# Kernel tuning notes

Hardware: AMD Instinct MI355X
Metric: run time of the kernel (lower is better)

The kernel has to match this reference:

```python
import jax, jax.numpy as jnp
import numpy as np

TEMPERATURE = 0.07
EPS = 1e-8
LAMBDA_CONTRASTIVE = 0.3
AMBIGUOUS_THRESHOLD = 0.05
LABEL_SMOOTHING = 0.1

B, D, NUM_DIMS, NUM_PIECES = 4096, 256, 19, 1024


def setup_inputs() -> dict:
    key = jax.random.key(0)
    ks = jax.random.split(key, 7)
    return {
        "z_a": jax.random.normal(ks[0], (B, D), dtype=jnp.float32),
        "z_b": jax.random.normal(ks[1], (B, D), dtype=jnp.float32),
        "ranking_logits": jax.random.normal(ks[2], (B, NUM_DIMS), dtype=jnp.float32),
        "labels_a": jax.random.uniform(ks[3], (B, NUM_DIMS), dtype=jnp.float32),
        "labels_b": jax.random.uniform(ks[4], (B, NUM_DIMS), dtype=jnp.float32),
        "piece_ids_a": jax.random.randint(ks[5], (B,), 0, NUM_PIECES, dtype=jnp.int64 if jax.config.jax_enable_x64 else jnp.int32),
        "piece_ids_b": jax.random.randint(ks[6], (B,), 0, NUM_PIECES, dtype=jnp.int64 if jax.config.jax_enable_x64 else jnp.int32),
    }


def _infonce(embeddings, piece_ids, temperature=TEMPERATURE, eps=EPS):
    # embeddings [N, D], piece_ids [N]. Same-piece samples are positives.
    norm = jnp.sqrt(jnp.sum(embeddings * embeddings, axis=-1, keepdims=True))
    z = embeddings / jnp.maximum(norm, eps)  # F.normalize semantics
    sim = (z @ z.T) / temperature  # [N, N]
    n = sim.shape[0]
    eye = jnp.eye(n, dtype=bool)
    piece_mask = piece_ids[None, :] == piece_ids[:, None]
    pos_mask = piece_mask & ~eye
    neg_mask = (~piece_mask) & ~eye
    # row-wise max subtraction (detached in torch) is a no-op on the value since
    # (pos - logsumexp) is shift-invariant; compute stably via masked logsumexp.
    neg_inf = jnp.array(-jnp.inf, sim.dtype)
    neg_lse = jax.scipy.special.logsumexp(jnp.where(neg_mask, sim, neg_inf), axis=-1)  # [N]
    valid_anchor = pos_mask.any(axis=1) & neg_mask.any(axis=1)  # [N]
    pair_mask = pos_mask & valid_anchor[:, None]  # each positive of a valid anchor
    # per-positive term: logsumexp([pos_sim, negs_of_row]) - pos_sim
    lse = jnp.logaddexp(sim, neg_lse[:, None])  # [N, N]
    term = jnp.where(pair_mask, lse - sim, 0.0)
    count = jnp.sum(pair_mask)
    loss = jnp.sum(term) / jnp.maximum(count, 1)
    return jnp.where(count > 0, loss, 0.0)


def _ranking_loss(logits, labels_a, labels_b,
                  ambiguous_threshold=AMBIGUOUS_THRESHOLD,
                  label_smoothing=LABEL_SMOOTHING):
    label_diff = labels_a - labels_b
    targets = (label_diff > 0).astype(logits.dtype)
    non_ambiguous = jnp.abs(label_diff) >= ambiguous_threshold
    targets = targets * (1.0 - label_smoothing) + 0.5 * label_smoothing
    # BCE-with-logits, elementwise, mean over non-ambiguous entries
    bce = jnp.maximum(logits, 0.0) - logits * targets + jnp.log1p(jnp.exp(-jnp.abs(logits)))
    cnt = jnp.sum(non_ambiguous)
    loss = jnp.sum(jnp.where(non_ambiguous, bce, 0.0)) / jnp.maximum(cnt, 1)
    return jnp.where(cnt > 0, loss, 0.0)


def reference(z_a, z_b, ranking_logits, labels_a, labels_b, piece_ids_a, piece_ids_b):
    l_rank = _ranking_loss(ranking_logits, labels_a, labels_b)
    all_z = jnp.concatenate([z_a, z_b], axis=0)        # [2B, D]
    all_pieces = jnp.concatenate([piece_ids_a, piece_ids_b], axis=0)  # [2B]
    l_contrast = _infonce(all_z, all_pieces)
    total = l_rank + LAMBDA_CONTRASTIVE * l_contrast
    return (total, l_rank, l_contrast)
```

## Files before the change

### kernel.cpp

```cpp
#include <hip/hip_runtime.h>
#include <hip/hip_bf16.h>
#include <math.h>

#define NTOT 8192
#define HB   4096
#define DIM  256
#define RANK_N (4096*19)
#define INV_T 14.285714285714286f
#define SHIFT 16.0f
#define MAXP  48

typedef __attribute__((ext_vector_type(8))) short bf16x8_t;
typedef __attribute__((ext_vector_type(4))) float f32x4_t;

__device__ __forceinline__ unsigned short f2bf(float f) {
  union { float fv; unsigned int u; } v; v.fv = f;
  unsigned int u = v.u;
  unsigned int r = u + 0x7FFFu + ((u >> 16) & 1u);
  return (unsigned short)(r >> 16);
}

__device__ __forceinline__ const float* zrow(const float* za, const float* zb, int g) {
  return g < HB ? za + (size_t)g * DIM : zb + (size_t)(g - HB) * DIM;
}
__device__ __forceinline__ int piece_of(const int* pa, const int* pb, int g) {
  return g < HB ? pa[g] : pb[g - HB];
}

__global__ void k_norm(const float* __restrict__ za, const float* __restrict__ zb,
                       const int* __restrict__ pa, const int* __restrict__ pb,
                       unsigned short* __restrict__ zn, int* __restrict__ hist) {
  int lane = threadIdx.x & 63;
  int w = threadIdx.x >> 6;
  int row = blockIdx.x * 4 + w;
  const float* src = zrow(za, zb, row);
  float4 v = *reinterpret_cast<const float4*>(src + lane * 4);
  float ss = v.x * v.x + v.y * v.y + v.z * v.z + v.w * v.w;
  for (int o = 32; o; o >>= 1) ss += __shfl_xor(ss, o, 64);
  float inv = 1.0f / fmaxf(sqrtf(ss), 1e-8f);
  ushort4 o;
  o.x = f2bf(v.x * inv); o.y = f2bf(v.y * inv);
  o.z = f2bf(v.z * inv); o.w = f2bf(v.w * inv);
  *reinterpret_cast<ushort4*>(zn + (size_t)row * DIM + lane * 4) = o;
  if (lane == 0) atomicAdd(&hist[piece_of(pa, pb, row)], 1);
}

__global__ void k_rank(const float* __restrict__ logits, const float* __restrict__ la,
                       const float* __restrict__ lb, float* __restrict__ accf) {
  int e = blockIdx.x * 256 + threadIdx.x;
  float lsum = 0.f, lcnt = 0.f;
  float diff = la[e] - lb[e];
  if (fabsf(diff) >= 0.05f) {
    float x = logits[e];
    float tgt = diff > 0.f ? 0.95f : 0.05f;
    lsum = fmaxf(x, 0.f) - x * tgt + log1pf(__expf(-fabsf(x)));
    lcnt = 1.f;
  }
  for (int o = 32; o; o >>= 1) { lsum += __shfl_xor(lsum, o, 64); lcnt += __shfl_xor(lcnt, o, 64); }
  __shared__ float sred[8];
  int w = threadIdx.x >> 6, lane = threadIdx.x & 63;
  if (lane == 0) { sred[w * 2] = lsum; sred[w * 2 + 1] = lcnt; }
  __syncthreads();
  if (threadIdx.x == 0) {
    float S = 0.f, C = 0.f;
    for (int i = 0; i < 4; ++i) { S += sred[i * 2]; C += sred[i * 2 + 1]; }
    atomicAdd(&accf[0], S);
    atomicAdd(&accf[1], C);
  }
}

__global__ __launch_bounds__(256, 2)
void k_gram(const unsigned short* __restrict__ zn,
            const int* __restrict__ pa, const int* __restrict__ pb,
            float* __restrict__ neg_s, int* __restrict__ posCount,
            float* __restrict__ pos_sims) {
  __shared__ unsigned short Bs[64 * 264];
  const int t = threadIdx.x;
  const int lane = t & 63;
  const int w = t >> 6;
  const int l15 = lane & 15;
  const int lg = lane >> 4;
  const int it = blockIdx.x >> 3;
  const int chunk = blockIdx.x & 7;
  const int ibase = it * 128;
  const int jbase0 = chunk * 1024;

  bf16x8_t afrag[2][8];
  for (int mt = 0; mt < 2; ++mt) {
    int garow = ibase + w * 32 + mt * 16 + l15;
    const unsigned short* asrc = zn + (size_t)garow * DIM;
    for (int ks = 0; ks < 8; ++ks)
      afrag[mt][ks] = *reinterpret_cast<const bf16x8_t*>(asrc + lg * 8 + ks * 32);
  }

  int prow[8], irow[8];
  for (int mt = 0; mt < 2; ++mt)
    for (int r = 0; r < 4; ++r) {
      int g = ibase + w * 32 + mt * 16 + lg * 4 + r;
      irow[mt * 4 + r] = g;
      prow[mt * 4 + r] = piece_of(pa, pb, g);
    }

  float s[8] = {0.f, 0.f, 0.f, 0.f, 0.f, 0.f, 0.f, 0.f};

  for (int jt = 0; jt < 16; ++jt) {
    int jb = jbase0 + jt * 64;
    __syncthreads();
    for (int i = 0; i < 8; ++i) {
      int f = t + i * 256;
      int r = f >> 5;
      int c = f & 31;
      bf16x8_t v = *reinterpret_cast<const bf16x8_t*>(zn + (size_t)(jb + r) * DIM + c * 8);
      *reinterpret_cast<bf16x8_t*>(&Bs[r * 264 + c * 8]) = v;
    }
    __syncthreads();
    for (int ct = 0; ct < 4; ++ct) {
      int jj = jb + ct * 16 + l15;
      int pc = piece_of(pa, pb, jj);
      int brow = ct * 16 + l15;
      f32x4_t acc0 = {0.f, 0.f, 0.f, 0.f};
      f32x4_t acc1 = {0.f, 0.f, 0.f, 0.f};
      for (int ks = 0; ks < 8; ++ks) {
        bf16x8_t bfrag = *reinterpret_cast<const bf16x8_t*>(&Bs[brow * 264 + lg * 8 + ks * 32]);
        acc0 = __builtin_amdgcn_mfma_f32_16x16x32_bf16(afrag[0][ks], bfrag, acc0, 0, 0, 0);
        acc1 = __builtin_amdgcn_mfma_f32_16x16x32_bf16(afrag[1][ks], bfrag, acc1, 0, 0, 0);
      }
      for (int r = 0; r < 4; ++r) {
        float sim0 = acc0[r] * INV_T;
        if (pc != prow[r]) {
          s[r] += __expf(sim0 - SHIFT);
        } else if (jj != irow[r]) {
          int slot = atomicAdd(&posCount[irow[r]], 1);
          if (slot < MAXP) pos_sims[(size_t)irow[r] * MAXP + slot] = sim0;
        }
        float sim1 = acc1[r] * INV_T;
        if (pc != prow[4 + r]) {
          s[4 + r] += __expf(sim1 - SHIFT);
        } else if (jj != irow[4 + r]) {
          int slot = atomicAdd(&posCount[irow[4 + r]], 1);
          if (slot < MAXP) pos_sims[(size_t)irow[4 + r] * MAXP + slot] = sim1;
        }
      }
    }
  }
  for (int q = 0; q < 8; ++q) {
    float v = s[q];
    v += __shfl_xor(v, 1, 64);
    v += __shfl_xor(v, 2, 64);
    v += __shfl_xor(v, 4, 64);
    v += __shfl_xor(v, 8, 64);
    if (l15 == 0) atomicAdd(&neg_s[irow[q]], v);
  }
}

__global__ void k_pos2(const int* __restrict__ pa, const int* __restrict__ pb,
                       const int* __restrict__ hist, const float* __restrict__ neg_s,
                       const int* __restrict__ posCount, const float* __restrict__ pos_sims,
                       float* __restrict__ accf) {
  int i = blockIdx.x * 256 + threadIdx.x;
  float lsum = 0.f, lcnt = 0.f;
  int pi = piece_of(pa, pb, i);
  int cnt = hist[pi];
  if (cnt - 1 > 0 && NTOT - cnt > 0) {
    float nlse = SHIFT + logf(neg_s[i]);
    int m = posCount[i];
    if (m > MAXP) m = MAXP;
    for (int s = 0; s < m; ++s) {
      float sim = pos_sims[(size_t)i * MAXP + s];
      float x = nlse - sim;
      lsum += fmaxf(x, 0.f) + log1pf(__expf(-fabsf(x)));
    }
    lcnt = (float)(cnt - 1);
  }
  for (int o = 32; o; o >>= 1) { lsum += __shfl_xor(lsum, o, 64); lcnt += __shfl_xor(lcnt, o, 64); }
  int lane = threadIdx.x & 63;
  if (lane == 0) {
    atomicAdd(&accf[2], lsum);
    atomicAdd(&accf[3], lcnt);
  }
}

__global__ void k_final(const float* __restrict__ accf, float* __restrict__ out) {
  float rs = accf[0], rc = accf[1], ps = accf[2], pc = accf[3];
  float l_rank = rc > 0.f ? rs / rc : 0.f;
  float l_con = pc > 0.f ? ps / pc : 0.f;
  out[0] = l_rank + 0.3f * l_con;
  out[1] = l_rank;
  out[2] = l_con;
}

extern "C" void kernel_launch(void* const* d_in, const int* in_sizes, int n_in,
                              void* d_out, int out_size, void* d_ws, size_t ws_size,
                              hipStream_t stream) {
  const float* za     = (const float*)d_in[0];
  const float* zb     = (const float*)d_in[1];
  const float* logits = (const float*)d_in[2];
  const float* la     = (const float*)d_in[3];
  const float* lb     = (const float*)d_in[4];
  const int*   pa     = (const int*)d_in[5];
  const int*   pb     = (const int*)d_in[6];
  float* out = (float*)d_out;

  float* wsf = (float*)d_ws;
  int*   wsi = (int*)d_ws;
  float* neg_s    = wsf + 4;
  int*   hist     = wsi + 4 + NTOT;
  int*   posCount = wsi + 4 + NTOT + 1024;
  float* pos_sims = wsf + 4 + NTOT + 1024 + NTOT;
  unsigned short* zn = (unsigned short*)(wsf + 4 + NTOT + 1024 + NTOT + (size_t)NTOT * MAXP);

  hipMemsetAsync(d_ws, 0, (size_t)(4 + NTOT + 1024 + NTOT) * 4, stream);
  k_norm<<<NTOT / 4, 256, 0, stream>>>(za, zb, pa, pb, zn, hist);
  k_rank<<<RANK_N / 256, 256, 0, stream>>>(logits, la, lb, wsf);
  k_gram<<<512, 256, 0, stream>>>(zn, pa, pb, neg_s, posCount, pos_sims);
  k_pos2<<<NTOT / 256, 256, 0, stream>>>(pa, pb, hist, neg_s, posCount, pos_sims, wsf);
  k_final<<<1, 1, 0, stream>>>(wsf, out);
}
```

Before: 189.6 us.

## Merge small kernels, swizzle LDS, cache piece ids, double gram grid

Fuses the norm and ranking kernels into one launch, and merges the positive-pair reduction with the final combine into a single one-block kernel, cutting five launches to three. The gram kernel now splits columns into 16 chunks so it launches 1024 blocks, with launch bounds raised to 4 blocks per CU. Its LDS tile drops the padding in favour of an XOR swizzle, and column piece ids are cached in shared memory instead of read from global memory per tile. It also recomputes row indices instead of holding them in registers. The post kernel runs in one block and loops serially over 8192 rows, which may cost more than it saves.

After: 377.9 us. +99.3%, slower.

```diff
diff --git a/kernel.cpp b/kernel.cpp
--- a/kernel.cpp
+++ b/kernel.cpp
@@ -6,6 +6,8 @@
 #define HB   4096
 #define DIM  256
 #define RANK_N (4096*19)
+#define NORM_BLOCKS (NTOT/4)
+#define RANK_BLOCKS (RANK_N/256)
 #define INV_T 14.285714285714286f
 #define SHIFT 16.0f
 #define MAXP  48
@@ -27,63 +29,70 @@
   return g < HB ? pa[g] : pb[g - HB];
 }
 
-__global__ void k_norm(const float* __restrict__ za, const float* __restrict__ zb,
-                       const int* __restrict__ pa, const int* __restrict__ pb,
-                       unsigned short* __restrict__ zn, int* __restrict__ hist) {
-  int lane = threadIdx.x & 63;
-  int w = threadIdx.x >> 6;
-  int row = blockIdx.x * 4 + w;
-  const float* src = zrow(za, zb, row);
-  float4 v = *reinterpret_cast<const float4*>(src + lane * 4);
-  float ss = v.x * v.x + v.y * v.y + v.z * v.z + v.w * v.w;
-  for (int o = 32; o; o >>= 1) ss += __shfl_xor(ss, o, 64);
-  float inv = 1.0f / fmaxf(sqrtf(ss), 1e-8f);
-  ushort4 o;
-  o.x = f2bf(v.x * inv); o.y = f2bf(v.y * inv);
-  o.z = f2bf(v.z * inv); o.w = f2bf(v.w * inv);
-  *reinterpret_cast<ushort4*>(zn + (size_t)row * DIM + lane * 4) = o;
-  if (lane == 0) atomicAdd(&hist[piece_of(pa, pb, row)], 1);
-}
-
-__global__ void k_rank(const float* __restrict__ logits, const float* __restrict__ la,
-                       const float* __restrict__ lb, float* __restrict__ accf) {
-  int e = blockIdx.x * 256 + threadIdx.x;
-  float lsum = 0.f, lcnt = 0.f;
-  float diff = la[e] - lb[e];
-  if (fabsf(diff) >= 0.05f) {
-    float x = logits[e];
-    float tgt = diff > 0.f ? 0.95f : 0.05f;
-    lsum = fmaxf(x, 0.f) - x * tgt + log1pf(__expf(-fabsf(x)));
-    lcnt = 1.f;
-  }
-  for (int o = 32; o; o >>= 1) { lsum += __shfl_xor(lsum, o, 64); lcnt += __shfl_xor(lcnt, o, 64); }
+__global__ void k_pre(const float* __restrict__ za, const float* __restrict__ zb,
+                      const float* __restrict__ logits, const float* __restrict__ la,
+                      const float* __restrict__ lb,
+                      const int* __restrict__ pa, const int* __restrict__ pb,
+                      unsigned short* __restrict__ zn, int* __restrict__ hist,
+                      float* __restrict__ accf) {
   __shared__ float sred[8];
-  int w = threadIdx.x >> 6, lane = threadIdx.x & 63;
-  if (lane == 0) { sred[w * 2] = lsum; sred[w * 2 + 1] = lcnt; }
-  __syncthreads();
-  if (threadIdx.x == 0) {
-    float S = 0.f, C = 0.f;
-    for (int i = 0; i < 4; ++i) { S += sred[i * 2]; C += sred[i * 2 + 1]; }
-    atomicAdd(&accf[0], S);
-    atomicAdd(&accf[1], C);
-  }
-}
-
-__global__ __launch_bounds__(256, 2)
+  int bid = blockIdx.x;
+  int t = threadIdx.x;
+  if (bid < NORM_BLOCKS) {
+    int lane = t & 63, w = t >> 6;
+    int row = bid * 4 + w;
+    const float* src = zrow(za, zb, row);
+    float4 v = *reinterpret_cast<const float4*>(src + lane * 4);
+    float ss = v.x * v.x + v.y * v.y + v.z * v.z + v.w * v.w;
+    for (int o = 32; o; o >>= 1) ss += __shfl_xor(ss, o, 64);
+    float inv = 1.0f / fmaxf(sqrtf(ss), 1e-8f);
+    ushort4 o;
+    o.x = f2bf(v.x * inv); o.y = f2bf(v.y * inv);
+    o.z = f2bf(v.z * inv); o.w = f2bf(v.w * inv);
+    *reinterpret_cast<ushort4*>(zn + (size_t)row * DIM + lane * 4) = o;
+    if (lane == 0) atomicAdd(&hist[piece_of(pa, pb, row)], 1);
+  } else {
+    int e = (bid - NORM_BLOCKS) * 256 + t;
+    float lsum = 0.f, lcnt = 0.f;
+    float diff = la[e] - lb[e];
+    if (fabsf(diff) >= 0.05f) {
+      float x = logits[e];
+      float tgt = diff > 0.f ? 0.95f : 0.05f;
+      lsum = fmaxf(x, 0.f) - x * tgt + log1pf(__expf(-fabsf(x)));
+      lcnt = 1.f;
+    }
+    for (int o = 32; o; o >>= 1) { lsum += __shfl_xor(lsum, o, 64); lcnt += __shfl_xor(lcnt, o, 64); }
+    int w = t >> 6, lane = t & 63;
+    if (lane == 0) { sred[w * 2] = lsum; sred[w * 2 + 1] = lcnt; }
+    __syncthreads();
+    if (t == 0) {
+      float S = 0.f, C = 0.f;
+      for (int i = 0; i < 4; ++i) { S += sred[i * 2]; C += sred[i * 2 + 1]; }
+      atomicAdd(&accf[0], S);
+      atomicAdd(&accf[1], C);
+    }
+  }
+}
+
+__global__ __launch_bounds__(256, 4)
 void k_gram(const unsigned short* __restrict__ zn,
             const int* __restrict__ pa, const int* __restrict__ pb,
             float* __restrict__ neg_s, int* __restrict__ posCount,
             float* __restrict__ pos_sims) {
-  __shared__ unsigned short Bs[64 * 264];
+  __shared__ unsigned short Bs[64 * 256];
+  __shared__ int Ps[512];
   const int t = threadIdx.x;
   const int lane = t & 63;
   const int w = t >> 6;
   const int l15 = lane & 15;
   const int lg = lane >> 4;
-  const int it = blockIdx.x >> 3;
-  const int chunk = blockIdx.x & 7;
+  const int it = blockIdx.x >> 4;
+  const int chunk = blockIdx.x & 15;
   const int ibase = it * 128;
-  const int jbase0 = chunk * 1024;
+  const int jbase0 = chunk * 512;
+
+  Ps[t]       = piece_of(pa, pb, jbase0 + t);
+  Ps[t + 256] = piece_of(pa, pb, jbase0 + t + 256);
 
   bf16x8_t afrag[2][8];
   for (int mt = 0; mt < 2; ++mt) {
@@ -93,17 +102,14 @@
       afrag[mt][ks] = *reinterpret_cast<const bf16x8_t*>(asrc + lg * 8 + ks * 32);
   }
 
-  int prow[8], irow[8];
+  int prow[8];
   for (int mt = 0; mt < 2; ++mt)
-    for (int r = 0; r < 4; ++r) {
-      int g = ibase + w * 32 + mt * 16 + lg * 4 + r;
-      irow[mt * 4 + r] = g;
-      prow[mt * 4 + r] = piece_of(pa, pb, g);
-    }
+    for (int r = 0; r < 4; ++r)
+      prow[mt * 4 + r] = piece_of(pa, pb, ibase + w * 32 + mt * 16 + lg * 4 + r);
 
   float s[8] = {0.f, 0.f, 0.f, 0.f, 0.f, 0.f, 0.f, 0.f};
 
-  for (int jt = 0; jt < 16; ++jt) {
+  for (int jt = 0; jt < 8; ++jt) {
     int jb = jbase0 + jt * 64;
     __syncthreads();
     for (int i = 0; i < 8; ++i) {
@@ -111,34 +117,38 @@
       int r = f >> 5;
       int c = f & 31;
       bf16x8_t v = *reinterpret_cast<const bf16x8_t*>(zn + (size_t)(jb + r) * DIM + c * 8);
-      *reinterpret_cast<bf16x8_t*>(&Bs[r * 264 + c * 8]) = v;
+      *reinterpret_cast<bf16x8_t*>(&Bs[r * 256 + ((c * 8) ^ ((r & 7) << 3))]) = v;
     }
     __syncthreads();
     for (int ct = 0; ct < 4; ++ct) {
-      int jj = jb + ct * 16 + l15;
-      int pc = piece_of(pa, pb, jj);
+      int jl = jt * 64 + ct * 16 + l15;
+      int pc = Ps[jl];
+      int jj = jbase0 + jl;
       int brow = ct * 16 + l15;
       f32x4_t acc0 = {0.f, 0.f, 0.f, 0.f};
       f32x4_t acc1 = {0.f, 0.f, 0.f, 0.f};
       for (int ks = 0; ks < 8; ++ks) {
-        bf16x8_t bfrag = *reinterpret_cast<const bf16x8_t*>(&Bs[brow * 264 + lg * 8 + ks * 32]);
+        bf16x8_t bfrag = *reinterpret_cast<const bf16x8_t*>(
+            &Bs[brow * 256 + ((lg * 8 + ks * 32) ^ ((brow & 7) << 3))]);
         acc0 = __builtin_amdgcn_mfma_f32_16x16x32_bf16(afrag[0][ks], bfrag, acc0, 0, 0, 0);
         acc1 = __builtin_amdgcn_mfma_f32_16x16x32_bf16(afrag[1][ks], bfrag, acc1, 0, 0, 0);
       }
       for (int r = 0; r < 4; ++r) {
+        int gi0 = ibase + w * 32 + lg * 4 + r;
         float sim0 = acc0[r] * INV_T;
         if (pc != prow[r]) {
           s[r] += __expf(sim0 - SHIFT);
-        } else if (jj != irow[r]) {
-          int slot = atomicAdd(&posCount[irow[r]], 1);
-          if (slot < MAXP) pos_sims[(size_t)irow[r] * MAXP + slot] = sim0;
+        } else if (jj != gi0) {
+          int slot = atomicAdd(&posCount[gi0], 1);
+          if (slot < MAXP) pos_sims[(size_t)gi0 * MAXP + slot] = sim0;
         }
+        int gi1 = gi0 + 16;
         float sim1 = acc1[r] * INV_T;
         if (pc != prow[4 + r]) {
           s[4 + r] += __expf(sim1 - SHIFT);
-        } else if (jj != irow[4 + r]) {
-          int slot = atomicAdd(&posCount[irow[4 + r]], 1);
-          if (slot < MAXP) pos_sims[(size_t)irow[4 + r] * MAXP + slot] = sim1;
+        } else if (jj != gi1) {
+          int slot = atomicAdd(&posCount[gi1], 1);
+          if (slot < MAXP) pos_sims[(size_t)gi1 * MAXP + slot] = sim1;
         }
       }
     }
@@ -149,44 +159,45 @@
     v += __shfl_xor(v, 2, 64);
     v += __shfl_xor(v, 4, 64);
     v += __shfl_xor(v, 8, 64);
-    if (l15 == 0) atomicAdd(&neg_s[irow[q]], v);
-  }
-}
-
-__global__ void k_pos2(const int* __restrict__ pa, const int* __restrict__ pb,
+    if (l15 == 0)
+      atomicAdd(&neg_s[ibase + w * 32 + (q >> 2) * 16 + lg * 4 + (q & 3)], v);
+  }
+}
+
+__global__ void k_post(const int* __restrict__ pa, const int* __restrict__ pb,
                        const int* __restrict__ hist, const float* __restrict__ neg_s,
                        const int* __restrict__ posCount, const float* __restrict__ pos_sims,
-                       float* __restrict__ accf) {
-  int i = blockIdx.x * 256 + threadIdx.x;
+                       const float* __restrict__ accf, float* __restrict__ out) {
   float lsum = 0.f, lcnt = 0.f;
-  int pi = piece_of(pa, pb, i);
-  int cnt = hist[pi];
-  if (cnt - 1 > 0 && NTOT - cnt > 0) {
-    float nlse = SHIFT + logf(neg_s[i]);
-    int m = posCount[i];
-    if (m > MAXP) m = MAXP;
-    for (int s = 0; s < m; ++s) {
-      float sim = pos_sims[(size_t)i * MAXP + s];
-      float x = nlse - sim;
-      lsum += fmaxf(x, 0.f) + log1pf(__expf(-fabsf(x)));
-    }
-    lcnt = (float)(cnt - 1);
+  for (int i = threadIdx.x; i < NTOT; i += 256) {
+    int pi = piece_of(pa, pb, i);
+    int cnt = hist[pi];
+    if (cnt - 1 > 0 && NTOT - cnt > 0) {
+      float nlse = SHIFT + logf(neg_s[i]);
+      int m = posCount[i];
+      if (m > MAXP) m = MAXP;
+      for (int s = 0; s < m; ++s) {
+        float x = nlse - pos_sims[(size_t)i * MAXP + s];
+        lsum += fmaxf(x, 0.f) + log1pf(__expf(-fabsf(x)));
+      }
+      lcnt += (float)(cnt - 1);
+    }
   }
   for (int o = 32; o; o >>= 1) { lsum += __shfl_xor(lsum, o, 64); lcnt += __shfl_xor(lcnt, o, 64); }
-  int lane = threadIdx.x & 63;
-  if (lane == 0) {
-    atomicAdd(&accf[2], lsum);
-    atomicAdd(&accf[3], lcnt);
-  }
-}
-
-__global__ void k_final(const float* __restrict__ accf, float* __restrict__ out) {
-  float rs = accf[0], rc = accf[1], ps = accf[2], pc = accf[3];
-  float l_rank = rc > 0.f ? rs / rc : 0.f;
-  float l_con = pc > 0.f ? ps / pc : 0.f;
-  out[0] = l_rank + 0.3f * l_con;
-  out[1] = l_rank;
-  out[2] = l_con;
+  __shared__ float sred[8];
+  int w = threadIdx.x >> 6, lane = threadIdx.x & 63;
+  if (lane == 0) { sred[w * 2] = lsum; sred[w * 2 + 1] = lcnt; }
+  __syncthreads();
+  if (threadIdx.x == 0) {
+    float ps = 0.f, pcn = 0.f;
+    for (int i = 0; i < 4; ++i) { ps += sred[i * 2]; pcn += sred[i * 2 + 1]; }
+    float rs = accf[0], rc = accf[1];
+    float l_rank = rc > 0.f ? rs / rc : 0.f;
+    float l_con = pcn > 0.f ? ps / pcn : 0.f;
+    out[0] = l_rank + 0.3f * l_con;
+    out[1] = l_rank;
+    out[2] = l_con;
+  }
 }
 
 extern "C" void kernel_launch(void* const* d_in, const int* in_sizes, int n_in,
@@ -210,9 +221,7 @@
   unsigned short* zn = (unsigned short*)(wsf + 4 + NTOT + 1024 + NTOT + (size_t)NTOT * MAXP);
 
   hipMemsetAsync(d_ws, 0, (size_t)(4 + NTOT + 1024 + NTOT) * 4, stream);
-  k_norm<<<NTOT / 4, 256, 0, stream>>>(za, zb, pa, pb, zn, hist);
-  k_rank<<<RANK_N / 256, 256, 0, stream>>>(logits, la, lb, wsf);
-  k_gram<<<512, 256, 0, stream>>>(zn, pa, pb, neg_s, posCount, pos_sims);
-  k_pos2<<<NTOT / 256, 256, 0, stream>>>(pa, pb, hist, neg_s, posCount, pos_sims, wsf);
-  k_final<<<1, 1, 0, stream>>>(wsf, out);
-}
+  k_pre<<<NORM_BLOCKS + RANK_BLOCKS, 256, 0, stream>>>(za, zb, logits, la, lb, pa, pb, zn, hist, wsf);
+  k_gram<<<1024, 256, 0, stream>>>(zn, pa, pb, neg_s, posCount, pos_sims);
+  k_post<<<1, 256, 0, stream>>>(pa, pb, hist, neg_s, posCount, pos_sims, wsf, out);
+}
```
